# Kernel optimization log

Hardware: AMD Instinct MI355X
Metric: run time of the kernel (lower is better)

## Reference

```python
import jax, jax.numpy as jnp
import numpy as np

N_NODES = 1_000_000
NUM_GRAPHS = 512
IN_DIM = 128
ASSIGN_DIM = 128
N_EDGES = 2_000_000


def setup_inputs() -> dict:
    key = jax.random.key(0)
    kx, ke, kw1, kb1, kw2, kb2 = jax.random.split(key, 6)
    x = jax.random.normal(kx, (N_NODES, IN_DIM), dtype=jnp.float32)
    edge_index = jax.random.randint(ke, (2, N_EDGES), 0, N_NODES, dtype=jnp.int64)
    # sorted, contiguous graph ids covering all NUM_GRAPHS segments (equal sizes)
    batch = (jnp.arange(N_NODES, dtype=jnp.int64) * NUM_GRAPHS) // N_NODES
    W1 = jax.random.normal(kw1, (IN_DIM, ASSIGN_DIM), dtype=jnp.float32) * 0.02
    b1 = jax.random.normal(kb1, (ASSIGN_DIM,), dtype=jnp.float32) * 0.02
    W2 = jax.random.normal(kw2, (ASSIGN_DIM, ASSIGN_DIM), dtype=jnp.float32) * 0.02
    b2 = jax.random.normal(kb2, (ASSIGN_DIM,), dtype=jnp.float32) * 0.02
    return {"x": x, "edge_index": edge_index, "batch": batch,
            "W1": W1, "b1": b1, "W2": W2, "b2": b2}


def reference(x, edge_index, batch, W1, b1, W2, b2):
    # assign_matrix: Linear(input_dim -> assign_dim)
    assign_score = x @ W1 + b1                      # [N, assign_dim]
    h = assign_score @ W2 + b2                      # [N, assign_dim]
    # per-graph mean pooling: single-pass segment sum / counts
    sums = jax.ops.segment_sum(h, batch, num_segments=NUM_GRAPHS)   # [B, assign_dim]
    counts = jax.ops.segment_sum(jnp.ones((h.shape[0],), dtype=h.dtype),
                                 batch, num_segments=NUM_GRAPHS)    # [B]
    pooled_x = sums / counts[:, None]
    return (pooled_x, edge_index, batch)
```

## Files before the change

kernel.cpp:

```cpp
#include <hip/hip_runtime.h>

#define DIM 128
#define NUM_GRAPHS 512

__global__ __launch_bounds__(256) void seg_sum_kernel(
    const float* __restrict__ x, const int* __restrict__ batch,
    float* __restrict__ sums, float* __restrict__ counts, int n_nodes)
{
    const int NODES_PER_GROUP = 64;
    int chunk = threadIdx.x & 31;
    int group = threadIdx.x >> 5;
    long long node0 = (long long)blockIdx.x * 512 + (long long)group * NODES_PER_GROUP;
    const float4* __restrict__ xv = (const float4*)x;

    float4 acc = make_float4(0.f, 0.f, 0.f, 0.f);
    int cur_g = -1;
    float run = 0.f;

    for (int i = 0; i < NODES_PER_GROUP; ++i) {
        long long node = node0 + i;
        if (node >= n_nodes) break;
        int g = batch[node];
        if (g != cur_g) {
            if (cur_g >= 0) {
                float* s = sums + (long long)cur_g * DIM + chunk * 4;
                atomicAdd(s + 0, acc.x); atomicAdd(s + 1, acc.y);
                atomicAdd(s + 2, acc.z); atomicAdd(s + 3, acc.w);
                if (chunk == 0) atomicAdd(counts + cur_g, run);
            }
            cur_g = g;
            acc = make_float4(0.f, 0.f, 0.f, 0.f);
            run = 0.f;
        }
        float4 v = xv[node * 32 + chunk];
        acc.x += v.x; acc.y += v.y; acc.z += v.z; acc.w += v.w;
        run += 1.f;
    }
    if (cur_g >= 0) {
        float* s = sums + (long long)cur_g * DIM + chunk * 4;
        atomicAdd(s + 0, acc.x); atomicAdd(s + 1, acc.y);
        atomicAdd(s + 2, acc.z); atomicAdd(s + 3, acc.w);
        if (chunk == 0) atomicAdd(counts + cur_g, run);
    }
}

__global__ __launch_bounds__(DIM) void mlp_kernel(
    const float* __restrict__ sums, const float* __restrict__ counts,
    const float* __restrict__ W1, const float* __restrict__ b1,
    const float* __restrict__ W2, const float* __restrict__ b2,
    float* __restrict__ out)
{
    __shared__ float xrow[DIM];
    __shared__ float yrow[DIM];
    int g = blockIdx.x;
    int t = threadIdx.x;
    float inv_cnt = 1.0f / counts[g];
    xrow[t] = sums[(long long)g * DIM + t] * inv_cnt;
    __syncthreads();
    float acc = b1[t];
    #pragma unroll 8
    for (int k = 0; k < DIM; ++k) acc += xrow[k] * W1[k * DIM + t];
    yrow[t] = acc;
    __syncthreads();
    float acc2 = b2[t];
    #pragma unroll 8
    for (int k = 0; k < DIM; ++k) acc2 += yrow[k] * W2[k * DIM + t];
    out[(long long)g * DIM + t] = acc2;
}

__global__ __launch_bounds__(256) void copy_i2f(
    const int* __restrict__ src, float* __restrict__ dst, long long n)
{
    long long i4 = (long long)blockIdx.x * blockDim.x + threadIdx.x;
    long long n4 = n >> 2;
    if (i4 < n4) {
        int4 v = ((const int4*)src)[i4];
        ((float4*)dst)[i4] = make_float4((float)v.x, (float)v.y, (float)v.z, (float)v.w);
    }
    if (i4 == 0) {
        for (long long j = n4 << 2; j < n; ++j) dst[j] = (float)src[j];
    }
}

extern "C" void kernel_launch(void* const* d_in, const int* in_sizes, int n_in,
                              void* d_out, int out_size, void* d_ws, size_t ws_size,
                              hipStream_t stream) {
    const float* x     = (const float*)d_in[0];
    const int*   edge  = (const int*)d_in[1];
    const int*   batch = (const int*)d_in[2];
    const float* W1    = (const float*)d_in[3];
    const float* b1    = (const float*)d_in[4];
    const float* W2    = (const float*)d_in[5];
    const float* b2    = (const float*)d_in[6];
    float* out = (float*)d_out;

    long long edge_n  = in_sizes[1];
    long long n_nodes = in_sizes[2];

    float* sums   = (float*)d_ws;
    float* counts = sums + (size_t)NUM_GRAPHS * DIM;

    hipMemsetAsync(d_ws, 0, ((size_t)NUM_GRAPHS * DIM + NUM_GRAPHS) * sizeof(float), stream);

    int blocksA = (int)((n_nodes + 511) / 512);
    seg_sum_kernel<<<blocksA, 256, 0, stream>>>(x, batch, sums, counts, (int)n_nodes);

    mlp_kernel<<<NUM_GRAPHS, DIM, 0, stream>>>(sums, counts, W1, b1, W2, b2, out);

    float* edge_out  = out + (size_t)NUM_GRAPHS * DIM;
    float* batch_out = edge_out + edge_n;
    {
        long long n4 = edge_n >> 2;
        int blocks = (int)((n4 + 255) / 256);
        copy_i2f<<<blocks, 256, 0, stream>>>(edge, edge_out, edge_n);
    }
    {
        long long n4 = n_nodes >> 2;
        int blocks = (int)((n4 + 255) / 256);
        copy_i2f<<<blocks, 256, 0, stream>>>(batch, batch_out, n_nodes);
    }
}
```

Baseline: 715.4 us.

## Fast-path segment sums for sorted batch and fuse index copy kernels

The segment-sum kernel now reads only the first and last batch id of each 64-node group. When they match, it streams the rows with nontemporal loads into two independent accumulators. When the group spans exactly two graphs, it binary-searches for the boundary; otherwise it falls back to the old per-node loop. This removes the per-node batch load and branch from the inner loop of the bandwidth-bound reduction, but the fast path relies on batch being sorted. The two int-to-float copy launches are merged into one kernel, which drops the scalar tail handling for lengths not divisible by four.

```diff
diff --git a/kernel.cpp b/kernel.cpp
--- a/kernel.cpp
+++ b/kernel.cpp
@@ -3,44 +3,73 @@
 #define DIM 128
 #define NUM_GRAPHS 512
 
+typedef float f4 __attribute__((ext_vector_type(4)));
+
+__device__ __forceinline__ void flush_acc(float* __restrict__ sums,
+                                          float* __restrict__ counts,
+                                          int g, int chunk, f4 a, float run) {
+    float* s = sums + (size_t)g * DIM + chunk * 4;
+    atomicAdd(s + 0, a[0]); atomicAdd(s + 1, a[1]);
+    atomicAdd(s + 2, a[2]); atomicAdd(s + 3, a[3]);
+    if (chunk == 0) atomicAdd(counts + g, run);
+}
+
 __global__ __launch_bounds__(256) void seg_sum_kernel(
     const float* __restrict__ x, const int* __restrict__ batch,
     float* __restrict__ sums, float* __restrict__ counts, int n_nodes)
 {
-    const int NODES_PER_GROUP = 64;
+    const int NPT = 64;
     int chunk = threadIdx.x & 31;
     int group = threadIdx.x >> 5;
-    long long node0 = (long long)blockIdx.x * 512 + (long long)group * NODES_PER_GROUP;
-    const float4* __restrict__ xv = (const float4*)x;
+    long long node0 = (long long)blockIdx.x * 512 + (long long)group * NPT;
+    if (node0 >= n_nodes) return;
+    int cnt = NPT;
+    if (node0 + NPT > n_nodes) cnt = (int)(n_nodes - node0);
 
-    float4 acc = make_float4(0.f, 0.f, 0.f, 0.f);
-    int cur_g = -1;
-    float run = 0.f;
+    const f4* __restrict__ xv = (const f4*)x;
+    const f4* __restrict__ p = xv + node0 * 32 + chunk;
 
-    for (int i = 0; i < NODES_PER_GROUP; ++i) {
-        long long node = node0 + i;
-        if (node >= n_nodes) break;
-        int g = batch[node];
-        if (g != cur_g) {
-            if (cur_g >= 0) {
-                float* s = sums + (long long)cur_g * DIM + chunk * 4;
-                atomicAdd(s + 0, acc.x); atomicAdd(s + 1, acc.y);
-                atomicAdd(s + 2, acc.z); atomicAdd(s + 3, acc.w);
-                if (chunk == 0) atomicAdd(counts + cur_g, run);
+    int g0 = batch[node0];
+    int g1 = batch[node0 + cnt - 1];
+
+    if (g0 == g1) {
+        f4 a = (f4)0.f, b = (f4)0.f;
+        int i = 0;
+        #pragma unroll 4
+        for (; i + 1 < cnt; i += 2) {
+            f4 v0 = __builtin_nontemporal_load(p + (long long)i * 32);
+            f4 v1 = __builtin_nontemporal_load(p + (long long)(i + 1) * 32);
+            a += v0; b += v1;
+        }
+        if (i < cnt) a += __builtin_nontemporal_load(p + (long long)i * 32);
+        flush_acc(sums, counts, g0, chunk, a + b, (float)cnt);
+    } else if (g1 - g0 == 1) {
+        int lo = 1, hi = cnt - 1;
+        while (lo < hi) {
+            int mid = (lo + hi) >> 1;
+            if (batch[node0 + mid] == g0) lo = mid + 1; else hi = mid;
+        }
+        f4 a = (f4)0.f;
+        for (int i = 0; i < lo; ++i)
+            a += __builtin_nontemporal_load(p + (long long)i * 32);
+        flush_acc(sums, counts, g0, chunk, a, (float)lo);
+        a = (f4)0.f;
+        for (int i = lo; i < cnt; ++i)
+            a += __builtin_nontemporal_load(p + (long long)i * 32);
+        flush_acc(sums, counts, g1, chunk, a, (float)(cnt - lo));
+    } else {
+        f4 a = (f4)0.f;
+        int cur = g0; float run = 0.f;
+        for (int i = 0; i < cnt; ++i) {
+            int g = batch[node0 + i];
+            if (g != cur) {
+                flush_acc(sums, counts, cur, chunk, a, run);
+                cur = g; a = (f4)0.f; run = 0.f;
             }
-            cur_g = g;
-            acc = make_float4(0.f, 0.f, 0.f, 0.f);
-            run = 0.f;
+            a += __builtin_nontemporal_load(p + (long long)i * 32);
+            run += 1.f;
         }
-        float4 v = xv[node * 32 + chunk];
-        acc.x += v.x; acc.y += v.y; acc.z += v.z; acc.w += v.w;
-        run += 1.f;
-    }
-    if (cur_g >= 0) {
-        float* s = sums + (long long)cur_g * DIM + chunk * 4;
-        atomicAdd(s + 0, acc.x); atomicAdd(s + 1, acc.y);
-        atomicAdd(s + 2, acc.z); atomicAdd(s + 3, acc.w);
-        if (chunk == 0) atomicAdd(counts + cur_g, run);
+        flush_acc(sums, counts, cur, chunk, a, run);
     }
 }
 
@@ -55,7 +84,7 @@
     int g = blockIdx.x;
     int t = threadIdx.x;
     float inv_cnt = 1.0f / counts[g];
-    xrow[t] = sums[(long long)g * DIM + t] * inv_cnt;
+    xrow[t] = sums[(size_t)g * DIM + t] * inv_cnt;
     __syncthreads();
     float acc = b1[t];
     #pragma unroll 8
@@ -65,20 +94,23 @@
     float acc2 = b2[t];
     #pragma unroll 8
     for (int k = 0; k < DIM; ++k) acc2 += yrow[k] * W2[k * DIM + t];
-    out[(long long)g * DIM + t] = acc2;
+    out[(size_t)g * DIM + t] = acc2;
 }
 
-__global__ __launch_bounds__(256) void copy_i2f(
-    const int* __restrict__ src, float* __restrict__ dst, long long n)
+__global__ __launch_bounds__(256) void copy2_i2f(
+    const int4* __restrict__ e, float4* __restrict__ eo, long long ne4,
+    const int4* __restrict__ b, float4* __restrict__ bo, long long nb4)
 {
-    long long i4 = (long long)blockIdx.x * blockDim.x + threadIdx.x;
-    long long n4 = n >> 2;
-    if (i4 < n4) {
-        int4 v = ((const int4*)src)[i4];
-        ((float4*)dst)[i4] = make_float4((float)v.x, (float)v.y, (float)v.z, (float)v.w);
-    }
-    if (i4 == 0) {
-        for (long long j = n4 << 2; j < n; ++j) dst[j] = (float)src[j];
+    long long i = (long long)blockIdx.x * blockDim.x + threadIdx.x;
+    if (i < ne4) {
+        int4 v = e[i];
+        eo[i] = make_float4((float)v.x, (float)v.y, (float)v.z, (float)v.w);
+    } else {
+        long long j = i - ne4;
+        if (j < nb4) {
+            int4 v = b[j];
+            bo[j] = make_float4((float)v.x, (float)v.y, (float)v.z, (float)v.w);
+        }
     }
 }
 
@@ -109,14 +141,8 @@
 
     float* edge_out  = out + (size_t)NUM_GRAPHS * DIM;
     float* batch_out = edge_out + edge_n;
-    {
-        long long n4 = edge_n >> 2;
-        int blocks = (int)((n4 + 255) / 256);
-        copy_i2f<<<blocks, 256, 0, stream>>>(edge, edge_out, edge_n);
-    }
-    {
-        long long n4 = n_nodes >> 2;
-        int blocks = (int)((n4 + 255) / 256);
-        copy_i2f<<<blocks, 256, 0, stream>>>(batch, batch_out, n_nodes);
-    }
+    long long ne4 = edge_n >> 2, nb4 = n_nodes >> 2;
+    int blocksC = (int)((ne4 + nb4 + 255) / 256);
+    copy2_i2f<<<blocksC, 256, 0, stream>>>((const int4*)edge, (float4*)edge_out, ne4,
+                                           (const int4*)batch, (float4*)batch_out, nb4);
 }
```

Result: no change. 702.5 us (-1.8%).
